# Optimization experiments

Hardware: AMD Instinct MI355X
Metric: run time of the kernel (lower is better)

The kernel has to match this reference:

```python
import jax, jax.numpy as jnp
import numpy as np
from jax import lax

# dims: S=seq_len, B=batch, D=word dim, HE=encoder hidden, HD=decoder hidden,
# E=atomic embedding dim, A=num_atomic, T=max_steps, SOS=start token id
S, B, D = 48, 64, 300
HE, HD, E, A, T, SOS = 300, 256, 50, 128, 50, 1


def _u(key, shape, scale):
    return jax.random.uniform(key, shape, jnp.float32, -scale, scale)


def setup_inputs() -> dict:
    key = jax.random.key(0)
    ks = iter(jax.random.split(key, 64))
    inp = {"word_vectors": jax.random.normal(next(ks), (S, B, D), jnp.float32)}
    se = 1.0 / np.sqrt(HE)
    for l, din in ((0, D), (1, 2 * HE)):
        for d in ("f", "b"):
            inp[f"e{l}{d}_Wih"] = _u(next(ks), (3 * HE, din), se)
            inp[f"e{l}{d}_Whh"] = _u(next(ks), (3 * HE, HE), se)
            inp[f"e{l}{d}_bih"] = _u(next(ks), (3 * HE,), se)
            inp[f"e{l}{d}_bhh"] = _u(next(ks), (3 * HE,), se)
    sd = 1.0 / np.sqrt(HD)
    for l, din in ((0, E), (1, HD)):
        inp[f"d{l}_Wih"] = _u(next(ks), (3 * HD, din), sd)
        inp[f"d{l}_Whh"] = _u(next(ks), (3 * HD, HD), sd)
        inp[f"d{l}_bih"] = _u(next(ks), (3 * HD,), sd)
        inp[f"d{l}_bhh"] = _u(next(ks), (3 * HD,), sd)
    emb = jax.random.normal(next(ks), (A, E), jnp.float32)
    inp["emb"] = emb.at[0].set(0.0)  # padding_idx=0
    inp["Wout"] = _u(next(ks), (A, HD), sd)
    inp["bout"] = _u(next(ks), (A,), sd)
    so = 1.0 / np.sqrt(D)
    inp["Wh0"] = _u(next(ks), (2 * HD, D), so)
    inp["bh0"] = _u(next(ks), (2 * HD,), so)
    return inp


def gru_cell(x, h, Wih, Whh, bih, bhh):
    # PyTorch GRU cell semantics
    gi = x @ Wih.T + bih
    gh = h @ Whh.T + bhh
    ir, iz, inn = jnp.split(gi, 3, axis=-1)
    hr, hz, hn = jnp.split(gh, 3, axis=-1)
    r = jax.nn.sigmoid(ir + hr)
    z = jax.nn.sigmoid(iz + hz)
    n = jnp.tanh(inn + r * hn)
    return (1.0 - z) * n + z * h


def gru_layer(xs, Wih, Whh, bih, bhh, reverse=False):
    # xs: [S, B, din] -> [S, B, H]; h0 = zeros (torch default)
    h0 = jnp.zeros((xs.shape[1], Whh.shape[1]), xs.dtype)
    def step(h, x):
        hn = gru_cell(x, h, Wih, Whh, bih, bhh)
        return hn, hn
    _, ys = lax.scan(step, h0, xs, reverse=reverse)
    return ys


def reference(word_vectors, e0f_Wih, e0f_Whh, e0f_bih, e0f_bhh, e0b_Wih, e0b_Whh, e0b_bih, e0b_bhh, e1f_Wih, e1f_Whh, e1f_bih, e1f_bhh, e1b_Wih, e1b_Whh, e1b_bih, e1b_bhh, d0_Wih, d0_Whh, d0_bih, d0_bhh, d1_Wih, d1_Whh, d1_bih, d1_bhh, emb, Wout, bout, Wh0, bh0):
    # --- encoder: 2-layer bidirectional GRU (eval mode: no dropout) ---
    x0f = gru_layer(word_vectors, e0f_Wih, e0f_Whh, e0f_bih, e0f_bhh, reverse=False)
    x0b = gru_layer(word_vectors, e0b_Wih, e0b_Whh, e0b_bih, e0b_bhh, reverse=True)
    x0 = jnp.concatenate([x0f, x0b], axis=-1)  # [S,B,2*HE]
    x1f = gru_layer(x0, e1f_Wih, e1f_Whh, e1f_bih, e1f_bhh, reverse=False)
    x1b = gru_layer(x0, e1b_Wih, e1b_Whh, e1b_bih, e1b_bhh, reverse=True)
    enc = x1f + x1b  # view(S,B,2,HE).sum(dim=2) of concat == sum of directions

    N = S * B
    h = jnp.tanh(enc @ Wh0.T + bh0).reshape(N, 2, HD)  # [N,2,HD]
    h0, h1 = h[:, 0], h[:, 1]
    e = jnp.broadcast_to(emb[SOS], (N, E))

    def step(carry, _):
        h0, h1, e = carry
        h0n = gru_cell(e, h0, d0_Wih, d0_Whh, d0_bih, d0_bhh)
        h1n = gru_cell(h0n, h1, d1_Wih, d1_Whh, d1_bih, d1_bhh)
        y = jax.nn.log_softmax(h1n @ Wout.T + bout, axis=-1)  # [N,A]
        p = jnp.argmax(y, axis=-1)
        return (h0n, h1n, emb[p]), y

    _, Y = lax.scan(step, (h0, h1, e), None, length=T)  # [T,N,A]
    return Y.reshape(T, S, B, A)[:-1]
```

## Files before the change

kernel.cpp:

```cpp
#include <hip/hip_runtime.h>
#include <math.h>

#define S_ 48
#define B_ 64
#define D_ 300
#define HE_ 300
#define HD_ 256
#define E_ 50
#define A_ 128
#define T_ 50
#define N_ (S_*B_)

__device__ __forceinline__ float sigm(float x){ return 1.0f/(1.0f + expf(-x)); }

template<int MODE>
__global__ __launch_bounds__(256)
void gemm_bias_kernel(const float* __restrict__ A, const float* __restrict__ A2,
                      const float* __restrict__ W,
                      const float* __restrict__ bias, float* __restrict__ C,
                      float* __restrict__ C2, int M, int N, int K)
{
  __shared__ float As[16][64];
  __shared__ float Ws[16][64];
  const int tid = threadIdx.x;
  const int bm = blockIdx.y * 64;
  const int bn = blockIdx.x * 64;
  const int tx = tid & 15, ty = tid >> 4;
  const int lr = tid >> 2;
  const int lk = (tid & 3) << 2;
  float acc[4][4] = {{0.f}};
  for (int kb = 0; kb < K; kb += 16) {
    {
      const int row = bm + lr;
      const int k = kb + lk;
      const float* ap = A + (size_t)row * K + k;
      float4 v = make_float4(0.f,0.f,0.f,0.f);
      if (k + 3 < K) v = *reinterpret_cast<const float4*>(ap);
      else {
        if (k   < K) v.x = ap[0];
        if (k+1 < K) v.y = ap[1];
        if (k+2 < K) v.z = ap[2];
        if (k+3 < K) v.w = ap[3];
      }
      if (MODE == 2) {
        const float* ap2 = A2 + (size_t)row * K + k;
        if (k + 3 < K) {
          float4 v2 = *reinterpret_cast<const float4*>(ap2);
          v.x += v2.x; v.y += v2.y; v.z += v2.z; v.w += v2.w;
        } else {
          if (k   < K) v.x += ap2[0];
          if (k+1 < K) v.y += ap2[1];
          if (k+2 < K) v.z += ap2[2];
          if (k+3 < K) v.w += ap2[3];
        }
      }
      As[lk][lr]=v.x; As[lk+1][lr]=v.y; As[lk+2][lr]=v.z; As[lk+3][lr]=v.w;
    }
    {
      const int col = bn + lr;
      const int k = kb + lk;
      float4 v = make_float4(0.f,0.f,0.f,0.f);
      if (col < N) {
        const float* wp = W + (size_t)col * K + k;
        if (k + 3 < K) v = *reinterpret_cast<const float4*>(wp);
        else {
          if (k   < K) v.x = wp[0];
          if (k+1 < K) v.y = wp[1];
          if (k+2 < K) v.z = wp[2];
          if (k+3 < K) v.w = wp[3];
        }
      }
      Ws[lk][lr]=v.x; Ws[lk+1][lr]=v.y; Ws[lk+2][lr]=v.z; Ws[lk+3][lr]=v.w;
    }
    __syncthreads();
    #pragma unroll
    for (int kk = 0; kk < 16; ++kk) {
      float4 a4 = *reinterpret_cast<const float4*>(&As[kk][ty<<2]);
      float4 w4 = *reinterpret_cast<const float4*>(&Ws[kk][tx<<2]);
      const float* a = reinterpret_cast<const float*>(&a4);
      const float* w = reinterpret_cast<const float*>(&w4);
      #pragma unroll
      for (int i = 0; i < 4; ++i)
        #pragma unroll
        for (int j = 0; j < 4; ++j)
          acc[i][j] = fmaf(a[i], w[j], acc[i][j]);
    }
    __syncthreads();
  }
  #pragma unroll
  for (int i = 0; i < 4; ++i) {
    const int m = bm + (ty<<2) + i;
    #pragma unroll
    for (int j = 0; j < 4; ++j) {
      const int n = bn + (tx<<2) + j;
      if (n < N) {
        float v = acc[i][j] + bias[n];
        if (MODE == 0) {
          C[(size_t)m*N + n] = v;
        } else {
          v = tanhf(v);
          if (n < HD_) C[(size_t)m*HD_ + n] = v;
          else         C2[(size_t)m*HD_ + (n-HD_)] = v;
        }
      }
    }
  }
}

__global__ __launch_bounds__(256)
void transpose_kernel(const float* __restrict__ in, float* __restrict__ out,
                      int NC, int NK, int NKP)
{
  int idx = blockIdx.x * 256 + threadIdx.x;
  if (idx < NC*NKP) {
    int cI = idx / NKP, kI = idx % NKP;
    out[(size_t)kI*NC + cI] = (kI < NK) ? in[(size_t)cI*NK + kI] : 0.0f;
  }
}

template<int LAYER>
__global__ __launch_bounds__(640, 2)
void enc_layer_persistent(const float* __restrict__ gi_f, const float* __restrict__ gi_b,
                          const float* __restrict__ WhhT_f, const float* __restrict__ WhhT_b,
                          const float* __restrict__ bhh_f, const float* __restrict__ bhh_b,
                          float* __restrict__ out, float* __restrict__ outB)
{
  const int dir = blockIdx.y;
  const float* gi  = dir ? gi_b   : gi_f;
  const float* WT  = dir ? WhhT_b : WhhT_f;
  const float* bhh = dir ? bhh_b  : bhh_f;
  float* o = (LAYER == 1 && dir) ? outB : out;

  __shared__ float hA[4][304];
  __shared__ float hB[4][304];
  const int tid = threadIdx.x;
  const int half = tid / 320;
  const int j = tid - half*320;
  const int R0 = blockIdx.x * 4;
  const int r0 = half * 2;
  const bool act = (j < HE_);

  float b_r = 0.f, b_z = 0.f, b_n = 0.f;
  if (act) { b_r = bhh[j]; b_z = bhh[HE_+j]; b_n = bhh[2*HE_+j]; }
  __syncthreads();

  for (int t = 0; t < S_; ++t) {
    const int tt = dir ? (S_-1 - t) : t;
    float (*hin)[304]  = (t & 1) ? hB : hA;
    float (*hout)[304] = (t & 1) ? hA : hB;
    float ar[2]={0,0}, az[2]={0,0}, an[2]={0,0};
    if (act && t > 0) {
      for (int k = 0; k < HE_; k += 4) {
        float wr[4], wz[4], wn[4];
        #pragma unroll
        for (int u = 0; u < 4; ++u) {
          const float* wk = WT + (size_t)(k+u)*(3*HE_);
          wr[u] = wk[j]; wz[u] = wk[HE_+j]; wn[u] = wk[2*HE_+j];
        }
        #pragma unroll
        for (int r = 0; r < 2; ++r) {
          float4 h4 = *reinterpret_cast<const float4*>(&hin[r0+r][k]);
          ar[r]=fmaf(h4.x,wr[0],ar[r]); ar[r]=fmaf(h4.y,wr[1],ar[r]);
          ar[r]=fmaf(h4.z,wr[2],ar[r]); ar[r]=fmaf(h4.w,wr[3],ar[r]);
          az[r]=fmaf(h4.x,wz[0],az[r]); az[r]=fmaf(h4.y,wz[1],az[r]);
          az[r]=fmaf(h4.z,wz[2],az[r]); az[r]=fmaf(h4.w,wz[3],az[r]);
          an[r]=fmaf(h4.x,wn[0],an[r]); an[r]=fmaf(h4.y,wn[1],an[r]);
          an[r]=fmaf(h4.z,wn[2],an[r]); an[r]=fmaf(h4.w,wn[3],an[r]);
        }
      }
    }
    if (act) {
      #pragma unroll
      for (int r = 0; r < 2; ++r) {
        const int row = R0 + r0 + r;
        const size_t gb = (size_t)(tt*B_ + row) * (3*HE_);
        float gr = gi[gb + j];
        float gz = gi[gb + HE_ + j];
        float gn = gi[gb + 2*HE_ + j];
        float rg = sigm(gr + ar[r] + b_r);
        float zg = sigm(gz + az[r] + b_z);
        float ng = tanhf(gn + rg*(an[r] + b_n));
        float ho = (t > 0) ? hin[r0+r][j] : 0.0f;
        float hn = (1.0f - zg)*ng + zg*ho;
        hout[r0+r][j] = hn;
        if (LAYER == 0) o[(size_t)(tt*B_ + row)*(2*HE_) + dir*HE_ + j] = hn;
        else            o[(size_t)(tt*B_ + row)*HE_ + j] = hn;
      }
    }
    __syncthreads();
  }
}

__global__ __launch_bounds__(1024, 4)
void dec_persistent(const float* __restrict__ WihT0,
                    const float* __restrict__ WhhT0,
                    const float* __restrict__ WihT1,
                    const float* __restrict__ WhhT1,
                    const float* __restrict__ WoutT,
                    const float* __restrict__ bih0, const float* __restrict__ bhh0,
                    const float* __restrict__ bih1, const float* __restrict__ bhh1,
                    const float* __restrict__ bout,
                    const float* __restrict__ emb,
                    const float* __restrict__ h0init, const float* __restrict__ h1init,
                    float* __restrict__ Y)
{
  __shared__ float h0s[12][256];
  __shared__ float h1s[12][256];
  __shared__ float es[12][52];
  const int tid = threadIdx.x;
  const int R0 = blockIdx.x * 12;
  const int c  = tid & 255;
  const int q  = tid >> 8;
  const int r0 = q * 3;

  for (int i = tid; i < 12*64; i += 1024) {
    int r = i >> 6, k = (i & 63) << 2;
    *reinterpret_cast<float4*>(&h0s[r][k]) =
        *reinterpret_cast<const float4*>(&h0init[(size_t)(R0+r)*HD_ + k]);
    *reinterpret_cast<float4*>(&h1s[r][k]) =
        *reinterpret_cast<const float4*>(&h1init[(size_t)(R0+r)*HD_ + k]);
  }
  for (int i = tid; i < 12*52; i += 1024) {
    int r = i / 52, k = i - r*52;
    es[r][k] = (k < E_) ? emb[E_ + k] : 0.0f;
  }
  const float b0r = bih0[c] + bhh0[c];
  const float b0z = bih0[HD_+c] + bhh0[HD_+c];
  const float b0ni = bih0[2*HD_+c];
  const float b0nh = bhh0[2*HD_+c];
  const float b1r = bih1[c] + bhh1[c];
  const float b1z = bih1[HD_+c] + bhh1[HD_+c];
  const float b1ni = bih1[2*HD_+c];
  const float b1nh = bhh1[2*HD_+c];
  const float bo0 = bout[tid & 63];
  const float bo1 = bout[64 + (tid & 63)];
  __syncthreads();

  for (int s = 0; s < T_-1; ++s) {
    float ar[3]={0,0,0}, az[3]={0,0,0}, ani[3]={0,0,0}, anh[3]={0,0,0};
    for (int kq = 0; kq < 64; ++kq) {
      const int k = kq << 2;
      float wr[4], wz[4], wn[4];
      #pragma unroll
      for (int u = 0; u < 4; ++u) {
        const float* wk = WhhT0 + (size_t)(k+u)*768;
        wr[u]=wk[c]; wz[u]=wk[256+c]; wn[u]=wk[512+c];
      }
      #pragma unroll
      for (int r = 0; r < 3; ++r) {
        float4 x = *reinterpret_cast<const float4*>(&h0s[r0+r][k]);
        ar[r]=fmaf(x.x,wr[0],ar[r]); ar[r]=fmaf(x.y,wr[1],ar[r]);
        ar[r]=fmaf(x.z,wr[2],ar[r]); ar[r]=fmaf(x.w,wr[3],ar[r]);
        az[r]=fmaf(x.x,wz[0],az[r]); az[r]=fmaf(x.y,wz[1],az[r]);
        az[r]=fmaf(x.z,wz[2],az[r]); az[r]=fmaf(x.w,wz[3],az[r]);
        anh[r]=fmaf(x.x,wn[0],anh[r]); anh[r]=fmaf(x.y,wn[1],anh[r]);
        anh[r]=fmaf(x.z,wn[2],anh[r]); anh[r]=fmaf(x.w,wn[3],anh[r]);
      }
      if (kq < 13) {
        float vr[4], vz[4], vn[4];
        #pragma unroll
        for (int u = 0; u < 4; ++u) {
          const float* wk = WihT0 + (size_t)(k+u)*768;
          vr[u]=wk[c]; vz[u]=wk[256+c]; vn[u]=wk[512+c];
        }
        #pragma unroll
        for (int r = 0; r < 3; ++r) {
          float4 e = *reinterpret_cast<const float4*>(&es[r0+r][k]);
          ar[r]=fmaf(e.x,vr[0],ar[r]); ar[r]=fmaf(e.y,vr[1],ar[r]);
          ar[r]=fmaf(e.z,vr[2],ar[r]); ar[r]=fmaf(e.w,vr[3],ar[r]);
          az[r]=fmaf(e.x,vz[0],az[r]); az[r]=fmaf(e.y,vz[1],az[r]);
          az[r]=fmaf(e.z,vz[2],az[r]); az[r]=fmaf(e.w,vz[3],az[r]);
          ani[r]=fmaf(e.x,vn[0],ani[r]); ani[r]=fmaf(e.y,vn[1],ani[r]);
          ani[r]=fmaf(e.z,vn[2],ani[r]); ani[r]=fmaf(e.w,vn[3],ani[r]);
        }
      }
    }
    __syncthreads();
    {
      float hnew[3];
      #pragma unroll
      for (int r = 0; r < 3; ++r) {
        float rg = sigm(ar[r] + b0r);
        float zg = sigm(az[r] + b0z);
        float ng = tanhf(ani[r] + b0ni + rg*(anh[r] + b0nh));
        float hold = h0s[r0+r][c];
        hnew[r] = (1.0f - zg)*ng + zg*hold;
      }
      #pragma unroll
      for (int r = 0; r < 3; ++r) h0s[r0+r][c] = hnew[r];
    }
    __syncthreads();
    #pragma unroll
    for (int r = 0; r < 3; ++r) { ar[r]=0.f; az[r]=0.f; ani[r]=0.f; anh[r]=0.f; }
    for (int kq = 0; kq < 64; ++kq) {
      const int k = kq << 2;
      float vr[4], vz[4], vn[4], wr[4], wz[4], wn[4];
      #pragma unroll
      for (int u = 0; u < 4; ++u) {
        const float* wk  = WihT1 + (size_t)(k+u)*768;
        vr[u]=wk[c]; vz[u]=wk[256+c]; vn[u]=wk[512+c];
        const float* wk2 = WhhT1 + (size_t)(k+u)*768;
        wr[u]=wk2[c]; wz[u]=wk2[256+c]; wn[u]=wk2[512+c];
      }
      #pragma unroll
      for (int r = 0; r < 3; ++r) {
        float4 x = *reinterpret_cast<const float4*>(&h0s[r0+r][k]);
        ar[r]=fmaf(x.x,vr[0],ar[r]); ar[r]=fmaf(x.y,vr[1],ar[r]);
        ar[r]=fmaf(x.z,vr[2],ar[r]); ar[r]=fmaf(x.w,vr[3],ar[r]);
        az[r]=fmaf(x.x,vz[0],az[r]); az[r]=fmaf(x.y,vz[1],az[r]);
        az[r]=fmaf(x.z,vz[2],az[r]); az[r]=fmaf(x.w,vz[3],az[r]);
        ani[r]=fmaf(x.x,vn[0],ani[r]); ani[r]=fmaf(x.y,vn[1],ani[r]);
        ani[r]=fmaf(x.z,vn[2],ani[r]); ani[r]=fmaf(x.w,vn[3],ani[r]);
        float4 y = *reinterpret_cast<const float4*>(&h1s[r0+r][k]);
        ar[r]=fmaf(y.x,wr[0],ar[r]); ar[r]=fmaf(y.y,wr[1],ar[r]);
        ar[r]=fmaf(y.z,wr[2],ar[r]); ar[r]=fmaf(y.w,wr[3],ar[r]);
        az[r]=fmaf(y.x,wz[0],az[r]); az[r]=fmaf(y.y,wz[1],az[r]);
        az[r]=fmaf(y.z,wz[2],az[r]); az[r]=fmaf(y.w,wz[3],az[r]);
        anh[r]=fmaf(y.x,wn[0],anh[r]); anh[r]=fmaf(y.y,wn[1],anh[r]);
        anh[r]=fmaf(y.z,wn[2],anh[r]); anh[r]=fmaf(y.w,wn[3],anh[r]);
      }
    }
    __syncthreads();
    {
      float hnew[3];
      #pragma unroll
      for (int r = 0; r < 3; ++r) {
        float rg = sigm(ar[r] + b1r);
        float zg = sigm(az[r] + b1z);
        float ng = tanhf(ani[r] + b1ni + rg*(anh[r] + b1nh));
        float hold = h1s[r0+r][c];
        hnew[r] = (1.0f - zg)*ng + zg*hold;
      }
      #pragma unroll
      for (int r = 0; r < 3; ++r) h1s[r0+r][c] = hnew[r];
    }
    __syncthreads();
    {
      const int w = tid >> 6;
      const int lane = tid & 63;
      if (w < 12) {
        const int row = w;
        float a0 = 0.f, a1 = 0.f;
        for (int k = 0; k < HD_; k += 2) {
          float w00 = WoutT[(size_t)k*A_ + lane];
          float w01 = WoutT[(size_t)k*A_ + 64 + lane];
          float w10 = WoutT[(size_t)(k+1)*A_ + lane];
          float w11 = WoutT[(size_t)(k+1)*A_ + 64 + lane];
          float2 hv = *reinterpret_cast<const float2*>(&h1s[row][k]);
          a0 = fmaf(hv.x, w00, a0); a0 = fmaf(hv.y, w10, a0);
          a1 = fmaf(hv.x, w01, a1); a1 = fmaf(hv.y, w11, a1);
        }
        float v0 = a0 + bo0;
        float v1 = a1 + bo1;
        float mx = fmaxf(v0, v1);
        #pragma unroll
        for (int off = 32; off >= 1; off >>= 1) mx = fmaxf(mx, __shfl_xor(mx, off));
        float sum = expf(v0 - mx) + expf(v1 - mx);
        #pragma unroll
        for (int off = 32; off >= 1; off >>= 1) sum += __shfl_xor(sum, off);
        float lz = mx + logf(sum);
        float* Yr = Y + ((size_t)s*N_ + R0 + row)*A_;
        Yr[lane]      = v0 - lz;
        Yr[64 + lane] = v1 - lz;
        float bv; int bi;
        if (v0 >= v1) { bv = v0; bi = lane; } else { bv = v1; bi = 64 + lane; }
        #pragma unroll
        for (int off = 32; off >= 1; off >>= 1) {
          float ov = __shfl_xor(bv, off);
          int   oi = __shfl_xor(bi, off);
          if (ov > bv || (ov == bv && oi < bi)) { bv = ov; bi = oi; }
        }
        if (lane < E_) es[row][lane] = emb[(size_t)bi*E_ + lane];
      }
    }
    __syncthreads();
  }
}

extern "C" void kernel_launch(void* const* d_in, const int* in_sizes, int n_in,
                              void* d_out, int out_size, void* d_ws, size_t ws_size,
                              hipStream_t stream)
{
  (void)in_sizes; (void)n_in; (void)out_size; (void)ws_size;
  const float* wv      = (const float*)d_in[0];
  const float* e0f_Wih = (const float*)d_in[1];
  const float* e0f_Whh = (const float*)d_in[2];
  const float* e0f_bih = (const float*)d_in[3];
  const float* e0f_bhh = (const float*)d_in[4];
  const float* e0b_Wih = (const float*)d_in[5];
  const float* e0b_Whh = (const float*)d_in[6];
  const float* e0b_bih = (const float*)d_in[7];
  const float* e0b_bhh = (const float*)d_in[8];
  const float* e1f_Wih = (const float*)d_in[9];
  const float* e1f_Whh = (const float*)d_in[10];
  const float* e1f_bih = (const float*)d_in[11];
  const float* e1f_bhh = (const float*)d_in[12];
  const float* e1b_Wih = (const float*)d_in[13];
  const float* e1b_Whh = (const float*)d_in[14];
  const float* e1b_bih = (const float*)d_in[15];
  const float* e1b_bhh = (const float*)d_in[16];
  const float* d0_Wih  = (const float*)d_in[17];
  const float* d0_Whh  = (const float*)d_in[18];
  const float* d0_bih  = (const float*)d_in[19];
  const float* d0_bhh  = (const float*)d_in[20];
  const float* d1_Wih  = (const float*)d_in[21];
  const float* d1_Whh  = (const float*)d_in[22];
  const float* d1_bih  = (const float*)d_in[23];
  const float* d1_bhh  = (const float*)d_in[24];
  const float* emb     = (const float*)d_in[25];
  const float* Wout    = (const float*)d_in[26];
  const float* bout    = (const float*)d_in[27];
  const float* Wh0     = (const float*)d_in[28];
  const float* bh0     = (const float*)d_in[29];

  float* ws = (float*)d_ws;
  float* giA  = ws;
  float* giB  = giA + (size_t)N_*3*HE_;
  float* x0   = giB + (size_t)N_*3*HE_;
  float* eWhT = x0  + (size_t)N_*2*HE_;
  float* eT0f = eWhT;
  float* eT0b = eT0f + (size_t)3*HE_*HE_;
  float* eT1f = eT0b + (size_t)3*HE_*HE_;
  float* eT1b = eT1f + (size_t)3*HE_*HE_;
  float* encF = x0;
  float* encB = x0 + (size_t)N_*HE_;
  float* h0A  = giA;
  float* h1A  = giA + (size_t)N_*HD_;
  float* WihT0 = eWhT;
  float* WhhT0 = WihT0 + (size_t)52*768;
  float* WihT1 = WhhT0 + (size_t)HD_*768;
  float* WhhT1 = WihT1 + (size_t)HD_*768;
  float* WoutT = WhhT1 + (size_t)HD_*768;
  float* Y = (float*)d_out;

  const dim3 blk(256);

  transpose_kernel<<<dim3((3*HE_*HE_+255)/256), blk, 0, stream>>>(e0f_Whh, eT0f, 3*HE_, HE_, HE_);
  transpose_kernel<<<dim3((3*HE_*HE_+255)/256), blk, 0, stream>>>(e0b_Whh, eT0b, 3*HE_, HE_, HE_);
  transpose_kernel<<<dim3((3*HE_*HE_+255)/256), blk, 0, stream>>>(e1f_Whh, eT1f, 3*HE_, HE_, HE_);
  transpose_kernel<<<dim3((3*HE_*HE_+255)/256), blk, 0, stream>>>(e1b_Whh, eT1b, 3*HE_, HE_, HE_);
  gemm_bias_kernel<0><<<dim3(15,48), blk, 0, stream>>>(wv, nullptr, e0f_Wih, e0f_bih, giA, nullptr, N_, 3*HE_, D_);
  gemm_bias_kernel<0><<<dim3(15,48), blk, 0, stream>>>(wv, nullptr, e0b_Wih, e0b_bih, giB, nullptr, N_, 3*HE_, D_);
  enc_layer_persistent<0><<<dim3(16,2), dim3(640), 0, stream>>>(giA, giB, eT0f, eT0b, e0f_bhh, e0b_bhh, x0, nullptr);
  gemm_bias_kernel<0><<<dim3(15,48), blk, 0, stream>>>(x0, nullptr, e1f_Wih, e1f_bih, giA, nullptr, N_, 3*HE_, 2*HE_);
  gemm_bias_kernel<0><<<dim3(15,48), blk, 0, stream>>>(x0, nullptr, e1b_Wih, e1b_bih, giB, nullptr, N_, 3*HE_, 2*HE_);
  enc_layer_persistent<1><<<dim3(16,2), dim3(640), 0, stream>>>(giA, giB, eT1f, eT1b, e1f_bhh, e1b_bhh, encF, encB);
  transpose_kernel<<<dim3((768*52+255)/256),   blk, 0, stream>>>(d0_Wih, WihT0, 3*HD_, E_,  52);
  transpose_kernel<<<dim3((768*256+255)/256),  blk, 0, stream>>>(d0_Whh, WhhT0, 3*HD_, HD_, HD_);
  transpose_kernel<<<dim3((768*256+255)/256),  blk, 0, stream>>>(d1_Wih, WihT1, 3*HD_, HD_, HD_);
  transpose_kernel<<<dim3((768*256+255)/256),  blk, 0, stream>>>(d1_Whh, WhhT1, 3*HD_, HD_, HD_);
  transpose_kernel<<<dim3((128*256+255)/256),  blk, 0, stream>>>(Wout,   WoutT, A_,    HD_, HD_);
  gemm_bias_kernel<2><<<dim3(8,48), blk, 0, stream>>>(encF, encB, Wh0, bh0, h0A, h1A, N_, 2*HD_, HE_);
  dec_persistent<<<dim3(N_/12), dim3(1024), 0, stream>>>(
      WihT0, WhhT0, WihT1, WhhT1, WoutT,
      d0_bih, d0_bhh, d1_bih, d1_bhh, bout,
      emb, h0A, h1A, Y);
}
```

Baseline: 7.987 ms.

## Stage decoder GRU weights through double-buffered LDS tiles with packed layouts

The decoder's weights are repacked on the device into chunked, interleaved layouts: layer 0 merges Whh and Wih into 39 chunks, and layer 1 interleaves Wih and Whh. The persistent decoder kernel now streams these chunks through a double-buffered 96KB shared-memory tile, prefetching the next chunk into registers while computing on the current one. The block shrinks from 1024 to 512 threads, each handling 6 rows instead of 3. The goal is to turn scattered per-thread global weight loads into coalesced float4 tile loads and reuse each loaded weight across more rows. In exchange it uses much more LDS, adds a barrier per chunk, and likely lowers occupancy.

```diff
diff --git a/kernel.cpp b/kernel.cpp
--- a/kernel.cpp
+++ b/kernel.cpp
@@ -108,14 +108,37 @@
 }
 
 __global__ __launch_bounds__(256)
-void transpose_kernel(const float* __restrict__ in, float* __restrict__ out,
-                      int NC, int NK, int NKP)
+void ctranspose_kernel(const float* __restrict__ in, float* __restrict__ out,
+                       int NC, int NK, int NKP, int dstride, int row0, int coff)
 {
   int idx = blockIdx.x * 256 + threadIdx.x;
   if (idx < NC*NKP) {
-    int cI = idx / NKP, kI = idx % NKP;
-    out[(size_t)kI*NC + cI] = (kI < NK) ? in[(size_t)cI*NK + kI] : 0.0f;
-  }
+    int gc = idx / NKP, k = idx % NKP;
+    out[(size_t)(row0+k)*dstride + coff + gc] =
+        (k < NK) ? in[(size_t)gc*NK + k] : 0.0f;
+  }
+}
+
+__global__ __launch_bounds__(256)
+void pack_dec0_kernel(const float* __restrict__ Whh, const float* __restrict__ Wih,
+                      float* __restrict__ out)
+{
+  int idx = blockIdx.x * 256 + threadIdx.x;
+  if (idx >= 39*6144) return;
+  int t  = idx / 6144;
+  int w  = idx % 6144;
+  int rr = w / 768;
+  int gc = w % 768;
+  float v = 0.0f;
+  if (t < 13) {
+    int k = t*4 + (rr & 3);
+    if (rr < 4) v = Whh[(size_t)gc*HD_ + k];
+    else if (k < E_) v = Wih[(size_t)gc*E_ + k];
+  } else {
+    int k = 52 + (t-13)*8 + rr;
+    if (k < HD_) v = Whh[(size_t)gc*HD_ + k];
+  }
+  out[idx] = v;
 }
 
 template<int LAYER>
@@ -191,11 +214,9 @@
   }
 }
 
-__global__ __launch_bounds__(1024, 4)
-void dec_persistent(const float* __restrict__ WihT0,
-                    const float* __restrict__ WhhT0,
-                    const float* __restrict__ WihT1,
-                    const float* __restrict__ WhhT1,
+__global__ __launch_bounds__(512)
+void dec_persistent(const float* __restrict__ Wc0,
+                    const float* __restrict__ Wc1T,
                     const float* __restrict__ WoutT,
                     const float* __restrict__ bih0, const float* __restrict__ bhh0,
                     const float* __restrict__ bih1, const float* __restrict__ bhh1,
@@ -204,24 +225,27 @@
                     const float* __restrict__ h0init, const float* __restrict__ h1init,
                     float* __restrict__ Y)
 {
-  __shared__ float h0s[12][256];
-  __shared__ float h1s[12][256];
-  __shared__ float es[12][52];
+  __shared__ __align__(16) float wb[2][12288];
+  __shared__ __align__(16) float h0s[12][256];
+  __shared__ __align__(16) float h1s[12][256];
+  __shared__ __align__(16) float es[12][56];
   const int tid = threadIdx.x;
   const int R0 = blockIdx.x * 12;
   const int c  = tid & 255;
-  const int q  = tid >> 8;
-  const int r0 = q * 3;
-
-  for (int i = tid; i < 12*64; i += 1024) {
+  const int half = tid >> 8;
+  const int r0 = half * 6;
+  const int lane = tid & 63;
+  const int wave = tid >> 6;
+
+  for (int i = tid; i < 12*64; i += 512) {
     int r = i >> 6, k = (i & 63) << 2;
     *reinterpret_cast<float4*>(&h0s[r][k]) =
         *reinterpret_cast<const float4*>(&h0init[(size_t)(R0+r)*HD_ + k]);
     *reinterpret_cast<float4*>(&h1s[r][k]) =
         *reinterpret_cast<const float4*>(&h1init[(size_t)(R0+r)*HD_ + k]);
   }
-  for (int i = tid; i < 12*52; i += 1024) {
-    int r = i / 52, k = i - r*52;
+  for (int i = tid; i < 12*56; i += 512) {
+    int r = i / 56, k = i - r*56;
     es[r][k] = (k < E_) ? emb[E_ + k] : 0.0f;
   }
   const float b0r = bih0[c] + bhh0[c];
@@ -232,54 +256,108 @@
   const float b1z = bih1[HD_+c] + bhh1[HD_+c];
   const float b1ni = bih1[2*HD_+c];
   const float b1nh = bhh1[2*HD_+c];
-  const float bo0 = bout[tid & 63];
-  const float bo1 = bout[64 + (tid & 63)];
+  const float bo0 = bout[lane];
+  const float bo1 = bout[64 + lane];
   __syncthreads();
 
   for (int s = 0; s < T_-1; ++s) {
-    float ar[3]={0,0,0}, az[3]={0,0,0}, ani[3]={0,0,0}, anh[3]={0,0,0};
-    for (int kq = 0; kq < 64; ++kq) {
-      const int k = kq << 2;
-      float wr[4], wz[4], wn[4];
-      #pragma unroll
-      for (int u = 0; u < 4; ++u) {
-        const float* wk = WhhT0 + (size_t)(k+u)*768;
-        wr[u]=wk[c]; wz[u]=wk[256+c]; wn[u]=wk[512+c];
-      }
-      #pragma unroll
-      for (int r = 0; r < 3; ++r) {
-        float4 x = *reinterpret_cast<const float4*>(&h0s[r0+r][k]);
-        ar[r]=fmaf(x.x,wr[0],ar[r]); ar[r]=fmaf(x.y,wr[1],ar[r]);
-        ar[r]=fmaf(x.z,wr[2],ar[r]); ar[r]=fmaf(x.w,wr[3],ar[r]);
-        az[r]=fmaf(x.x,wz[0],az[r]); az[r]=fmaf(x.y,wz[1],az[r]);
-        az[r]=fmaf(x.z,wz[2],az[r]); az[r]=fmaf(x.w,wz[3],az[r]);
-        anh[r]=fmaf(x.x,wn[0],anh[r]); anh[r]=fmaf(x.y,wn[1],anh[r]);
-        anh[r]=fmaf(x.z,wn[2],anh[r]); anh[r]=fmaf(x.w,wn[3],anh[r]);
-      }
-      if (kq < 13) {
-        float vr[4], vz[4], vn[4];
-        #pragma unroll
-        for (int u = 0; u < 4; ++u) {
-          const float* wk = WihT0 + (size_t)(k+u)*768;
-          vr[u]=wk[c]; vz[u]=wk[256+c]; vn[u]=wk[512+c];
-        }
-        #pragma unroll
-        for (int r = 0; r < 3; ++r) {
-          float4 e = *reinterpret_cast<const float4*>(&es[r0+r][k]);
-          ar[r]=fmaf(e.x,vr[0],ar[r]); ar[r]=fmaf(e.y,vr[1],ar[r]);
-          ar[r]=fmaf(e.z,vr[2],ar[r]); ar[r]=fmaf(e.w,vr[3],ar[r]);
-          az[r]=fmaf(e.x,vz[0],az[r]); az[r]=fmaf(e.y,vz[1],az[r]);
-          az[r]=fmaf(e.z,vz[2],az[r]); az[r]=fmaf(e.w,vz[3],az[r]);
-          ani[r]=fmaf(e.x,vn[0],ani[r]); ani[r]=fmaf(e.y,vn[1],ani[r]);
-          ani[r]=fmaf(e.z,vn[2],ani[r]); ani[r]=fmaf(e.w,vn[3],ani[r]);
-        }
-      }
-    }
-    __syncthreads();
+    float ar[6]={0,0,0,0,0,0}, az[6]={0,0,0,0,0,0};
+    float ani[6]={0,0,0,0,0,0}, anh[6]={0,0,0,0,0,0};
+    #pragma unroll
+    for (int j = 0; j < 3; ++j) {
+      *reinterpret_cast<float4*>(&wb[0][(tid + j*512)*4]) =
+          *reinterpret_cast<const float4*>(Wc0 + (size_t)(tid + j*512)*4);
+    }
+    __syncthreads();
+    int cur = 0;
+    for (int t = 0; t < 39; ++t) {
+      float4 nv0, nv1, nv2;
+      if (t < 38) {
+        const float* src = Wc0 + (size_t)(t+1)*6144;
+        nv0 = *reinterpret_cast<const float4*>(src + (size_t)tid*4);
+        nv1 = *reinterpret_cast<const float4*>(src + (size_t)(tid+512)*4);
+        nv2 = *reinterpret_cast<const float4*>(src + (size_t)(tid+1024)*4);
+      }
+      const float* w = wb[cur];
+      if (t < 13) {
+        const int k0 = t*4;
+        {
+          float wr[4], wz[4], wn[4];
+          #pragma unroll
+          for (int u = 0; u < 4; ++u) {
+            wr[u] = w[u*768 + c];
+            wz[u] = w[u*768 + 256 + c];
+            wn[u] = w[u*768 + 512 + c];
+          }
+          #pragma unroll
+          for (int r = 0; r < 6; ++r) {
+            float4 x = *reinterpret_cast<const float4*>(&h0s[r0+r][k0]);
+            ar[r]=fmaf(x.x,wr[0],ar[r]); ar[r]=fmaf(x.y,wr[1],ar[r]);
+            ar[r]=fmaf(x.z,wr[2],ar[r]); ar[r]=fmaf(x.w,wr[3],ar[r]);
+            az[r]=fmaf(x.x,wz[0],az[r]); az[r]=fmaf(x.y,wz[1],az[r]);
+            az[r]=fmaf(x.z,wz[2],az[r]); az[r]=fmaf(x.w,wz[3],az[r]);
+            anh[r]=fmaf(x.x,wn[0],anh[r]); anh[r]=fmaf(x.y,wn[1],anh[r]);
+            anh[r]=fmaf(x.z,wn[2],anh[r]); anh[r]=fmaf(x.w,wn[3],anh[r]);
+          }
+        }
+        {
+          float vr[4], vz[4], vn[4];
+          #pragma unroll
+          for (int u = 0; u < 4; ++u) {
+            vr[u] = w[(4+u)*768 + c];
+            vz[u] = w[(4+u)*768 + 256 + c];
+            vn[u] = w[(4+u)*768 + 512 + c];
+          }
+          #pragma unroll
+          for (int r = 0; r < 6; ++r) {
+            float4 e = *reinterpret_cast<const float4*>(&es[r0+r][k0]);
+            ar[r]=fmaf(e.x,vr[0],ar[r]); ar[r]=fmaf(e.y,vr[1],ar[r]);
+            ar[r]=fmaf(e.z,vr[2],ar[r]); ar[r]=fmaf(e.w,vr[3],ar[r]);
+            az[r]=fmaf(e.x,vz[0],az[r]); az[r]=fmaf(e.y,vz[1],az[r]);
+            az[r]=fmaf(e.z,vz[2],az[r]); az[r]=fmaf(e.w,vz[3],az[r]);
+            ani[r]=fmaf(e.x,vn[0],ani[r]); ani[r]=fmaf(e.y,vn[1],ani[r]);
+            ani[r]=fmaf(e.z,vn[2],ani[r]); ani[r]=fmaf(e.w,vn[3],ani[r]);
+          }
+        }
+      } else {
+        const int k0 = 52 + (t-13)*8;
+        #pragma unroll
+        for (int hh = 0; hh < 2; ++hh) {
+          const int k = k0 + hh*4;
+          if (k < HD_) {
+            float wr[4], wz[4], wn[4];
+            #pragma unroll
+            for (int u = 0; u < 4; ++u) {
+              wr[u] = w[(hh*4+u)*768 + c];
+              wz[u] = w[(hh*4+u)*768 + 256 + c];
+              wn[u] = w[(hh*4+u)*768 + 512 + c];
+            }
+            #pragma unroll
+            for (int r = 0; r < 6; ++r) {
+              float4 x = *reinterpret_cast<const float4*>(&h0s[r0+r][k]);
+              ar[r]=fmaf(x.x,wr[0],ar[r]); ar[r]=fmaf(x.y,wr[1],ar[r]);
+              ar[r]=fmaf(x.z,wr[2],ar[r]); ar[r]=fmaf(x.w,wr[3],ar[r]);
+              az[r]=fmaf(x.x,wz[0],az[r]); az[r]=fmaf(x.y,wz[1],az[r]);
+              az[r]=fmaf(x.z,wz[2],az[r]); az[r]=fmaf(x.w,wz[3],az[r]);
+              anh[r]=fmaf(x.x,wn[0],anh[r]); anh[r]=fmaf(x.y,wn[1],anh[r]);
+              anh[r]=fmaf(x.z,wn[2],anh[r]); anh[r]=fmaf(x.w,wn[3],anh[r]);
+            }
+          }
+        }
+      }
+      if (t < 38) {
+        float* dst = wb[cur^1];
+        *reinterpret_cast<float4*>(&dst[(size_t)tid*4])        = nv0;
+        *reinterpret_cast<float4*>(&dst[(size_t)(tid+512)*4])  = nv1;
+        *reinterpret_cast<float4*>(&dst[(size_t)(tid+1024)*4]) = nv2;
+      }
+      __syncthreads();
+      cur ^= 1;
+    }
     {
-      float hnew[3];
-      #pragma unroll
-      for (int r = 0; r < 3; ++r) {
+      float hnew[6];
+      #pragma unroll
+      for (int r = 0; r < 6; ++r) {
         float rg = sigm(ar[r] + b0r);
         float zg = sigm(az[r] + b0z);
         float ng = tanhf(ani[r] + b0ni + rg*(anh[r] + b0nh));
@@ -287,44 +365,69 @@
         hnew[r] = (1.0f - zg)*ng + zg*hold;
       }
       #pragma unroll
-      for (int r = 0; r < 3; ++r) h0s[r0+r][c] = hnew[r];
+      for (int r = 0; r < 6; ++r) h0s[r0+r][c] = hnew[r];
     }
     __syncthreads();
     #pragma unroll
-    for (int r = 0; r < 3; ++r) { ar[r]=0.f; az[r]=0.f; ani[r]=0.f; anh[r]=0.f; }
-    for (int kq = 0; kq < 64; ++kq) {
-      const int k = kq << 2;
-      float vr[4], vz[4], vn[4], wr[4], wz[4], wn[4];
-      #pragma unroll
-      for (int u = 0; u < 4; ++u) {
-        const float* wk  = WihT1 + (size_t)(k+u)*768;
-        vr[u]=wk[c]; vz[u]=wk[256+c]; vn[u]=wk[512+c];
-        const float* wk2 = WhhT1 + (size_t)(k+u)*768;
-        wr[u]=wk2[c]; wz[u]=wk2[256+c]; wn[u]=wk2[512+c];
-      }
-      #pragma unroll
-      for (int r = 0; r < 3; ++r) {
-        float4 x = *reinterpret_cast<const float4*>(&h0s[r0+r][k]);
-        ar[r]=fmaf(x.x,vr[0],ar[r]); ar[r]=fmaf(x.y,vr[1],ar[r]);
-        ar[r]=fmaf(x.z,vr[2],ar[r]); ar[r]=fmaf(x.w,vr[3],ar[r]);
-        az[r]=fmaf(x.x,vz[0],az[r]); az[r]=fmaf(x.y,vz[1],az[r]);
-        az[r]=fmaf(x.z,vz[2],az[r]); az[r]=fmaf(x.w,vz[3],az[r]);
-        ani[r]=fmaf(x.x,vn[0],ani[r]); ani[r]=fmaf(x.y,vn[1],ani[r]);
-        ani[r]=fmaf(x.z,vn[2],ani[r]); ani[r]=fmaf(x.w,vn[3],ani[r]);
-        float4 y = *reinterpret_cast<const float4*>(&h1s[r0+r][k]);
-        ar[r]=fmaf(y.x,wr[0],ar[r]); ar[r]=fmaf(y.y,wr[1],ar[r]);
-        ar[r]=fmaf(y.z,wr[2],ar[r]); ar[r]=fmaf(y.w,wr[3],ar[r]);
-        az[r]=fmaf(y.x,wz[0],az[r]); az[r]=fmaf(y.y,wz[1],az[r]);
-        az[r]=fmaf(y.z,wz[2],az[r]); az[r]=fmaf(y.w,wz[3],az[r]);
-        anh[r]=fmaf(y.x,wn[0],anh[r]); anh[r]=fmaf(y.y,wn[1],anh[r]);
-        anh[r]=fmaf(y.z,wn[2],anh[r]); anh[r]=fmaf(y.w,wn[3],anh[r]);
-      }
-    }
-    __syncthreads();
+    for (int r = 0; r < 6; ++r) { ar[r]=0.f; az[r]=0.f; ani[r]=0.f; anh[r]=0.f; }
+    #pragma unroll
+    for (int j = 0; j < 6; ++j) {
+      *reinterpret_cast<float4*>(&wb[0][(tid + j*512)*4]) =
+          *reinterpret_cast<const float4*>(Wc1T + (size_t)(tid + j*512)*4);
+    }
+    __syncthreads();
+    cur = 0;
+    for (int t = 0; t < 32; ++t) {
+      float4 nv[6];
+      if (t < 31) {
+        const float* src = Wc1T + (size_t)(t+1)*12288;
+        #pragma unroll
+        for (int j = 0; j < 6; ++j)
+          nv[j] = *reinterpret_cast<const float4*>(src + (size_t)(tid + j*512)*4);
+      }
+      const float* w = wb[cur];
+      const int k0 = t*8;
+      #pragma unroll
+      for (int kk = 0; kk < 8; kk += 4) {
+        float vr[4], vz[4], vn[4], wr[4], wz[4], wn[4];
+        #pragma unroll
+        for (int u = 0; u < 4; ++u) {
+          const int base = (kk+u)*1536;
+          vr[u] = w[base + c];        vz[u] = w[base + 256 + c];
+          vn[u] = w[base + 512 + c];  wr[u] = w[base + 768 + c];
+          wz[u] = w[base + 1024 + c]; wn[u] = w[base + 1280 + c];
+        }
+        #pragma unroll
+        for (int r = 0; r < 6; ++r) {
+          float4 x = *reinterpret_cast<const float4*>(&h0s[r0+r][k0+kk]);
+          ar[r]=fmaf(x.x,vr[0],ar[r]); ar[r]=fmaf(x.y,vr[1],ar[r]);
+          ar[r]=fmaf(x.z,vr[2],ar[r]); ar[r]=fmaf(x.w,vr[3],ar[r]);
+          az[r]=fmaf(x.x,vz[0],az[r]); az[r]=fmaf(x.y,vz[1],az[r]);
+          az[r]=fmaf(x.z,vz[2],az[r]); az[r]=fmaf(x.w,vz[3],az[r]);
+          ani[r]=fmaf(x.x,vn[0],ani[r]); ani[r]=fmaf(x.y,vn[1],ani[r]);
+          ani[r]=fmaf(x.z,vn[2],ani[r]); ani[r]=fmaf(x.w,vn[3],ani[r]);
+          float4 y = *reinterpret_cast<const float4*>(&h1s[r0+r][k0+kk]);
+          ar[r]=fmaf(y.x,wr[0],ar[r]); ar[r]=fmaf(y.y,wr[1],ar[r]);
+          ar[r]=fmaf(y.z,wr[2],ar[r]); ar[r]=fmaf(y.w,wr[3],ar[r]);
+          az[r]=fmaf(y.x,wz[0],az[r]); az[r]=fmaf(y.y,wz[1],az[r]);
+          az[r]=fmaf(y.z,wz[2],az[r]); az[r]=fmaf(y.w,wz[3],az[r]);
+          anh[r]=fmaf(y.x,wn[0],anh[r]); anh[r]=fmaf(y.y,wn[1],anh[r]);
+          anh[r]=fmaf(y.z,wn[2],anh[r]); anh[r]=fmaf(y.w,wn[3],anh[r]);
+        }
+      }
+      if (t < 31) {
+        float* dst = wb[cur^1];
+        #pragma unroll
+        for (int j = 0; j < 6; ++j)
+          *reinterpret_cast<float4*>(&dst[(size_t)(tid + j*512)*4]) = nv[j];
+      }
+      __syncthreads();
+      cur ^= 1;
+    }
     {
-      float hnew[3];
-      #pragma unroll
-      for (int r = 0; r < 3; ++r) {
+      float hnew[6];
+      #pragma unroll
+      for (int r = 0; r < 6; ++r) {
         float rg = sigm(ar[r] + b1r);
         float zg = sigm(az[r] + b1z);
         float ng = tanhf(ani[r] + b1ni + rg*(anh[r] + b1nh));
@@ -332,46 +435,41 @@
         hnew[r] = (1.0f - zg)*ng + zg*hold;
       }
       #pragma unroll
-      for (int r = 0; r < 3; ++r) h1s[r0+r][c] = hnew[r];
-    }
-    __syncthreads();
-    {
-      const int w = tid >> 6;
-      const int lane = tid & 63;
-      if (w < 12) {
-        const int row = w;
-        float a0 = 0.f, a1 = 0.f;
-        for (int k = 0; k < HD_; k += 2) {
-          float w00 = WoutT[(size_t)k*A_ + lane];
-          float w01 = WoutT[(size_t)k*A_ + 64 + lane];
-          float w10 = WoutT[(size_t)(k+1)*A_ + lane];
-          float w11 = WoutT[(size_t)(k+1)*A_ + 64 + lane];
-          float2 hv = *reinterpret_cast<const float2*>(&h1s[row][k]);
-          a0 = fmaf(hv.x, w00, a0); a0 = fmaf(hv.y, w10, a0);
-          a1 = fmaf(hv.x, w01, a1); a1 = fmaf(hv.y, w11, a1);
-        }
-        float v0 = a0 + bo0;
-        float v1 = a1 + bo1;
-        float mx = fmaxf(v0, v1);
-        #pragma unroll
-        for (int off = 32; off >= 1; off >>= 1) mx = fmaxf(mx, __shfl_xor(mx, off));
-        float sum = expf(v0 - mx) + expf(v1 - mx);
-        #pragma unroll
-        for (int off = 32; off >= 1; off >>= 1) sum += __shfl_xor(sum, off);
-        float lz = mx + logf(sum);
-        float* Yr = Y + ((size_t)s*N_ + R0 + row)*A_;
-        Yr[lane]      = v0 - lz;
-        Yr[64 + lane] = v1 - lz;
-        float bv; int bi;
-        if (v0 >= v1) { bv = v0; bi = lane; } else { bv = v1; bi = 64 + lane; }
-        #pragma unroll
-        for (int off = 32; off >= 1; off >>= 1) {
-          float ov = __shfl_xor(bv, off);
-          int   oi = __shfl_xor(bi, off);
-          if (ov > bv || (ov == bv && oi < bi)) { bv = ov; bi = oi; }
-        }
-        if (lane < E_) es[row][lane] = emb[(size_t)bi*E_ + lane];
-      }
+      for (int r = 0; r < 6; ++r) h1s[r0+r][c] = hnew[r];
+    }
+    __syncthreads();
+    for (int rr = wave; rr < 12; rr += 8) {
+      float a0 = 0.f, a1 = 0.f;
+      for (int k = 0; k < HD_; k += 2) {
+        float w00 = WoutT[(size_t)k*A_ + lane];
+        float w01 = WoutT[(size_t)k*A_ + 64 + lane];
+        float w10 = WoutT[(size_t)(k+1)*A_ + lane];
+        float w11 = WoutT[(size_t)(k+1)*A_ + 64 + lane];
+        float2 hv = *reinterpret_cast<const float2*>(&h1s[rr][k]);
+        a0 = fmaf(hv.x, w00, a0); a0 = fmaf(hv.y, w10, a0);
+        a1 = fmaf(hv.x, w01, a1); a1 = fmaf(hv.y, w11, a1);
+      }
+      float v0 = a0 + bo0;
+      float v1 = a1 + bo1;
+      float mx = fmaxf(v0, v1);
+      #pragma unroll
+      for (int off = 32; off >= 1; off >>= 1) mx = fmaxf(mx, __shfl_xor(mx, off));
+      float sum = expf(v0 - mx) + expf(v1 - mx);
+      #pragma unroll
+      for (int off = 32; off >= 1; off >>= 1) sum += __shfl_xor(sum, off);
+      float lz = mx + logf(sum);
+      float* Yr = Y + ((size_t)s*N_ + R0 + rr)*A_;
+      Yr[lane]      = v0 - lz;
+      Yr[64 + lane] = v1 - lz;
+      float bv; int bi;
+      if (v0 >= v1) { bv = v0; bi = lane; } else { bv = v1; bi = 64 + lane; }
+      #pragma unroll
+      for (int off = 32; off >= 1; off >>= 1) {
+        float ov = __shfl_xor(bv, off);
+        int   oi = __shfl_xor(bi, off);
+        if (ov > bv || (ov == bv && oi < bi)) { bv = ov; bi = oi; }
+      }
+      if (lane < E_) es[rr][lane] = emb[(size_t)bi*E_ + lane];
     }
     __syncthreads();
   }
@@ -426,33 +524,30 @@
   float* encB = x0 + (size_t)N_*HE_;
   float* h0A  = giA;
   float* h1A  = giA + (size_t)N_*HD_;
-  float* WihT0 = eWhT;
-  float* WhhT0 = WihT0 + (size_t)52*768;
-  float* WihT1 = WhhT0 + (size_t)HD_*768;
-  float* WhhT1 = WihT1 + (size_t)HD_*768;
-  float* WoutT = WhhT1 + (size_t)HD_*768;
+  float* Wc0   = eWhT;
+  float* Wc1T  = Wc0 + (size_t)39*6144;
+  float* WoutT = Wc1T + (size_t)256*1536;
   float* Y = (float*)d_out;
 
   const dim3 blk(256);
 
-  transpose_kernel<<<dim3((3*HE_*HE_+255)/256), blk, 0, stream>>>(e0f_Whh, eT0f, 3*HE_, HE_, HE_);
-  transpose_kernel<<<dim3((3*HE_*HE_+255)/256), blk, 0, stream>>>(e0b_Whh, eT0b, 3*HE_, HE_, HE_);
-  transpose_kernel<<<dim3((3*HE_*HE_+255)/256), blk, 0, stream>>>(e1f_Whh, eT1f, 3*HE_, HE_, HE_);
-  transpose_kernel<<<dim3((3*HE_*HE_+255)/256), blk, 0, stream>>>(e1b_Whh, eT1b, 3*HE_, HE_, HE_);
+  ctranspose_kernel<<<dim3(1055), blk, 0, stream>>>(e0f_Whh, eT0f, 3*HE_, HE_, HE_, 3*HE_, 0, 0);
+  ctranspose_kernel<<<dim3(1055), blk, 0, stream>>>(e0b_Whh, eT0b, 3*HE_, HE_, HE_, 3*HE_, 0, 0);
+  ctranspose_kernel<<<dim3(1055), blk, 0, stream>>>(e1f_Whh, eT1f, 3*HE_, HE_, HE_, 3*HE_, 0, 0);
+  ctranspose_kernel<<<dim3(1055), blk, 0, stream>>>(e1b_Whh, eT1b, 3*HE_, HE_, HE_, 3*HE_, 0, 0);
   gemm_bias_kernel<0><<<dim3(15,48), blk, 0, stream>>>(wv, nullptr, e0f_Wih, e0f_bih, giA, nullptr, N_, 3*HE_, D_);
   gemm_bias_kernel<0><<<dim3(15,48), blk, 0, stream>>>(wv, nullptr, e0b_Wih, e0b_bih, giB, nullptr, N_, 3*HE_, D_);
   enc_layer_persistent<0><<<dim3(16,2), dim3(640), 0, stream>>>(giA, giB, eT0f, eT0b, e0f_bhh, e0b_bhh, x0, nullptr);
   gemm_bias_kernel<0><<<dim3(15,48), blk, 0, stream>>>(x0, nullptr, e1f_Wih, e1f_bih, giA, nullptr, N_, 3*HE_, 2*HE_);
   gemm_bias_kernel<0><<<dim3(15,48), blk, 0, stream>>>(x0, nullptr, e1b_Wih, e1b_bih, giB, nullptr, N_, 3*HE_, 2*HE_);
   enc_layer_persistent<1><<<dim3(16,2), dim3(640), 0, stream>>>(giA, giB, eT1f, eT1b, e1f_bhh, e1b_bhh, encF, encB);
-  transpose_kernel<<<dim3((768*52+255)/256),   blk, 0, stream>>>(d0_Wih, WihT0, 3*HD_, E_,  52);
-  transpose_kernel<<<dim3((768*256+255)/256),  blk, 0, stream>>>(d0_Whh, WhhT0, 3*HD_, HD_, HD_);
-  transpose_kernel<<<dim3((768*256+255)/256),  blk, 0, stream>>>(d1_Wih, WihT1, 3*HD_, HD_, HD_);
-  transpose_kernel<<<dim3((768*256+255)/256),  blk, 0, stream>>>(d1_Whh, WhhT1, 3*HD_, HD_, HD_);
-  transpose_kernel<<<dim3((128*256+255)/256),  blk, 0, stream>>>(Wout,   WoutT, A_,    HD_, HD_);
+  pack_dec0_kernel<<<dim3(936), blk, 0, stream>>>(d0_Whh, d0_Wih, Wc0);
+  ctranspose_kernel<<<dim3(768), blk, 0, stream>>>(d1_Wih, Wc1T, 3*HD_, HD_, HD_, 1536, 0, 0);
+  ctranspose_kernel<<<dim3(768), blk, 0, stream>>>(d1_Whh, Wc1T, 3*HD_, HD_, HD_, 1536, 0, 768);
+  ctranspose_kernel<<<dim3(128), blk, 0, stream>>>(Wout,   WoutT, A_,   HD_, HD_, 128, 0, 0);
   gemm_bias_kernel<2><<<dim3(8,48), blk, 0, stream>>>(encF, encB, Wh0, bh0, h0A, h1A, N_, 2*HD_, HE_);
-  dec_persistent<<<dim3(N_/12), dim3(1024), 0, stream>>>(
-      WihT0, WhhT0, WihT1, WhhT1, WoutT,
+  dec_persistent<<<dim3(N_/12), dim3(512), 0, stream>>>(
+      Wc0, Wc1T, WoutT,
       d0_bih, d0_bhh, d1_bih, d1_bhh, bout,
       emb, h0A, h1A, Y);
 }
```

Result: slower. 11.38 ms (+42.4%).
